# Kernel tuning notes

Hardware: AMD Instinct MI355X
Metric: run time of the kernel (lower is better)

The kernel has to match this reference:

```python
import jax, jax.numpy as jnp
import numpy as np

D_MODEL = 1024
N_HEADS = 16
LN_EPS = 1e-6  # flax LayerNorm default

def setup_inputs() -> dict:
    key = jax.random.key(0)
    k1, k2, k3 = jax.random.split(key, 3)
    B, S = 2, 2048
    x = jax.random.normal(k1, (B, S, D_MODEL), dtype=jnp.float32)
    W_qkv = jax.random.normal(k2, (D_MODEL, 3 * D_MODEL), dtype=jnp.float32) / np.sqrt(D_MODEL)
    W_out = jax.random.normal(k3, (D_MODEL, D_MODEL), dtype=jnp.float32) / np.sqrt(D_MODEL)
    q_scale = jnp.ones((D_MODEL,), dtype=jnp.float32)
    k_scale = jnp.ones((D_MODEL,), dtype=jnp.float32)
    return {"x": x, "W_qkv": W_qkv, "q_scale": q_scale, "k_scale": k_scale, "W_out": W_out}

def _layernorm(t, scale):
    mu = jnp.mean(t, axis=-1, keepdims=True)
    var = jnp.var(t, axis=-1, keepdims=True)
    return (t - mu) * jax.lax.rsqrt(var + LN_EPS) * scale

def reference(x, W_qkv, q_scale, k_scale, W_out):
    B, S, D = x.shape
    H = N_HEADS
    Hd = D // H
    # fused QKV projection (no bias)
    qkv = jnp.einsum('bsd,de->bse', x, W_qkv)
    q, k, v = jnp.split(qkv, 3, axis=-1)
    # QK-LayerNorm over full d_model (before head split), scale only
    q = _layernorm(q, q_scale)
    k = _layernorm(k, k_scale)
    # split heads: [b, s, h, hd]
    q = q.reshape(B, S, H, Hd)
    k = k.reshape(B, S, H, Hd)
    v = v.reshape(B, S, H, Hd)
    # eager attention with causal mask
    scores = jnp.einsum('bshd,bthd->bhst', q / jnp.sqrt(Hd).astype(q.dtype), k)  # [b,h,s,t]
    future = jnp.triu(jnp.ones((S, S), dtype=bool), 1)  # True on strictly-future positions
    scores = jnp.where(future[None, None, :, :], jnp.finfo(scores.dtype).min, scores)
    attn = jax.nn.softmax(scores, axis=-1)
    ctx = jnp.einsum('bhst,bthd->bshd', attn, v)
    out = jnp.einsum('bsd,de->bse', ctx.reshape(B, S, D), W_out)
    return out
```

## Files before the change

### kernel.cpp

```cpp
#include <hip/hip_runtime.h>
#include <cstdint>
#include <cstddef>

typedef __attribute__((ext_vector_type(8))) short short8;
typedef __attribute__((ext_vector_type(4))) float floatx4;

__device__ __forceinline__ float bf2f(unsigned short u) {
  union { unsigned int i; float f; } c; c.i = ((unsigned int)u) << 16; return c.f;
}
__device__ __forceinline__ unsigned short f2bf(float f) {
  union { float f; unsigned int i; } c; c.f = f;
  unsigned int r = c.i + 0x7fffu + ((c.i >> 16) & 1u);
  return (unsigned short)(r >> 16);
}
__device__ __forceinline__ unsigned int fbits(float f) {
  union { float f; unsigned int i; } c; c.f = f; return c.i;
}

__device__ __forceinline__ void glds16(const unsigned short* g, unsigned short* l) {
  __builtin_amdgcn_global_load_lds((const __attribute__((address_space(1))) void*)g,
                                   (__attribute__((address_space(3))) void*)l, 16, 0, 0);
}

__device__ __forceinline__ void tr_tile(const float* __restrict__ in,
                                        unsigned short* __restrict__ out,
                                        int R, int C, int bx, int by, int tid,
                                        unsigned short (*t)[33]) {
  const int cx = tid & 31, rl = tid >> 5;
#pragma unroll
  for (int i = 0; i < 4; ++i)
    t[rl + i * 8][cx] = f2bf(in[(size_t)(by * 32 + rl + i * 8) * C + bx * 32 + cx]);
  __syncthreads();
  const int oc = by * 32 + cx;
#pragma unroll
  for (int i = 0; i < 4; ++i)
    out[(size_t)(bx * 32 + rl + i * 8) * R + oc] = t[cx][rl + i * 8];
}

__global__ __launch_bounds__(256) void k_prep(const float* __restrict__ x,
                                              const float* __restrict__ Wq,
                                              const float* __restrict__ Wo,
                                              unsigned short* __restrict__ x_bf,
                                              unsigned short* __restrict__ WTq,
                                              unsigned short* __restrict__ WTo) {
  __shared__ unsigned short t[32][33];
  const int bid = blockIdx.x, tid = threadIdx.x;
  if (bid < 3072) {
    tr_tile(Wq, WTq, 1024, 3072, bid % 96, bid / 96, tid, t);
  } else if (bid < 4096) {
    int v = bid - 3072;
    tr_tile(Wo, WTo, 1024, 1024, v & 31, v >> 5, tid, t);
  } else {
    int i = (bid - 4096) * 256 + tid;
    float4 v = ((const float4*)x)[i];
    ushort4 o = { f2bf(v.x), f2bf(v.y), f2bf(v.z), f2bf(v.w) };
    ((ushort4*)x_bf)[i] = o;
  }
}

template <int MT, bool F32OUT>
__global__ __launch_bounds__(256) void k_gemm_bt(const unsigned short* __restrict__ A,
                                                 const unsigned short* __restrict__ BT,
                                                 void* __restrict__ Cout,
                                                 int M, int N, int K) {
  constexpr int NI = MT / 32;
  __shared__ unsigned short As[2][MT * 32];
  __shared__ unsigned short Bs[2][128 * 32];
  const int bm = blockIdx.x * MT, bn = blockIdx.y * 128;
  const int tid = threadIdx.x;
  const int wave = tid >> 6, lane = tid & 63;
  const int wm = (wave & 1) * (MT / 2), wn = (wave >> 1) * 64;
  const int lrow = lane & 15, lgrp = lane >> 4;
  floatx4 acc[NI][4] = {};

  const int lr4 = lane >> 2, lc8 = (lane & 3) * 8;
  const int br0 = wave * 32;
  const unsigned short* Bg0 = BT + (size_t)(bn + br0 + lr4) * K + lc8;
  const unsigned short* Bg1 = BT + (size_t)(bn + br0 + 16 + lr4) * K + lc8;
  const int ar0 = wave * (MT / 4);
  const unsigned short* Ag0 = A + (size_t)(bm + ar0 + lr4) * K + lc8;
  const unsigned short* Ag1 = A + (size_t)(bm + ar0 + 16 + lr4) * K + lc8;

  for (int k0 = 0; k0 < K; k0 += 64) {
#pragma unroll
    for (int u = 0; u < 2; ++u) {
      const int ko = k0 + u * 32;
      glds16(Ag0 + ko, &As[u][ar0 * 32]);
      if (MT == 128) glds16(Ag1 + ko, &As[u][(ar0 + 16) * 32]);
      glds16(Bg0 + ko, &Bs[u][br0 * 32]);
      glds16(Bg1 + ko, &Bs[u][(br0 + 16) * 32]);
    }
    __syncthreads();
#pragma unroll
    for (int u = 0; u < 2; ++u) {
      short8 a[NI], bfr[4];
#pragma unroll
      for (int i = 0; i < NI; ++i)
        a[i] = *(const short8*)&As[u][(wm + i * 16 + lrow) * 32 + lgrp * 8];
#pragma unroll
      for (int j = 0; j < 4; ++j)
        bfr[j] = *(const short8*)&Bs[u][(wn + j * 16 + lrow) * 32 + lgrp * 8];
#pragma unroll
      for (int i = 0; i < NI; ++i)
#pragma unroll
        for (int j = 0; j < 4; ++j)
          acc[i][j] = __builtin_amdgcn_mfma_f32_16x16x32_bf16(a[i], bfr[j], acc[i][j], 0, 0, 0);
    }
    __syncthreads();
  }
#pragma unroll
  for (int i = 0; i < NI; ++i)
#pragma unroll
    for (int j = 0; j < 4; ++j)
#pragma unroll
      for (int r = 0; r < 4; ++r) {
        int m = bm + wm + i * 16 + lgrp * 4 + r;
        int n = bn + wn + j * 16 + lrow;
        if (F32OUT)
          ((float*)Cout)[(size_t)m * N + n] = acc[i][j][r];
        else
          ((unsigned short*)Cout)[(size_t)m * N + n] = f2bf(acc[i][j][r]);
      }
}

__global__ __launch_bounds__(256) void k_lnv(const unsigned short* __restrict__ qkv,
                                             const float* __restrict__ q_scale,
                                             const float* __restrict__ k_scale,
                                             unsigned short* __restrict__ q_n,
                                             unsigned short* __restrict__ k_n,
                                             unsigned short* __restrict__ VT) {
  const int bid = blockIdx.x, tid = threadIdx.x;
  if (bid < 4096) {
    const int tok = bid;
    const int wave = tid >> 6, lane = tid & 63;
    __shared__ float red[2][4];
    const unsigned short* row = qkv + (size_t)tok * 3072;
#pragma unroll
    for (int seg = 0; seg < 2; ++seg) {
      const unsigned short* p  = row + seg * 1024;
      const float* sc = seg ? k_scale : q_scale;
      unsigned short* outp = (seg ? k_n : q_n) + (size_t)tok * 1024;
      ushort4 u = *(const ushort4*)&p[tid * 4];
      float xv[4] = { bf2f(u.x), bf2f(u.y), bf2f(u.z), bf2f(u.w) };
      float sum = xv[0] + xv[1] + xv[2] + xv[3];
      float sq  = xv[0]*xv[0] + xv[1]*xv[1] + xv[2]*xv[2] + xv[3]*xv[3];
      for (int off = 32; off; off >>= 1) {
        sum += __shfl_down(sum, off, 64);
        sq  += __shfl_down(sq,  off, 64);
      }
      if (lane == 0) { red[0][wave] = sum; red[1][wave] = sq; }
      __syncthreads();
      sum = red[0][0] + red[0][1] + red[0][2] + red[0][3];
      sq  = red[1][0] + red[1][1] + red[1][2] + red[1][3];
      __syncthreads();
      float mean = sum * (1.0f / 1024.0f);
      float var  = sq * (1.0f / 1024.0f) - mean * mean;
      float rstd = rsqrtf(var + 1e-6f);
      if (seg == 0) rstd *= 0.18033688011112042f;
      float4 su = *(const float4*)&sc[tid * 4];
      ushort4 o;
      o.x = f2bf((xv[0] - mean) * rstd * su.x);
      o.y = f2bf((xv[1] - mean) * rstd * su.y);
      o.z = f2bf((xv[2] - mean) * rstd * su.z);
      o.w = f2bf((xv[3] - mean) * rstd * su.w);
      *(ushort4*)&outp[tid * 4] = o;
    }
  } else {
    __shared__ unsigned short t[32][33];
    const int v = bid - 4096;
    const int bh = v & 31, b = bh >> 4, h = bh & 15;
    const int sy = (v >> 5) & 63, hx = v >> 11;
    const int cx = tid & 31, rl = tid >> 5;
#pragma unroll
    for (int i = 0; i < 4; ++i)
      t[rl + i * 8][cx] =
        qkv[(size_t)(b * 2048 + sy * 32 + rl + i * 8) * 3072 + 2048 + h * 64 + hx * 32 + cx];
    __syncthreads();
#pragma unroll
    for (int i = 0; i < 4; ++i)
      VT[((size_t)bh * 64 + hx * 32 + rl + i * 8) * 2048 + sy * 32 + cx] = t[cx][rl + i * 8];
  }
}


#define KS_STRIDE 72
#define VS_STRIDE 136
#define PS_STRIDE 136

#define MFMA_BF16 __builtin_amdgcn_mfma_f32_16x16x32_bf16

template <bool MASKED>
__device__ __forceinline__ void attn_step(int t0, int q0, int wq, int wt,
    const short8 (&qa)[2][2],
    const unsigned short* Ks, const unsigned short* Vs, unsigned short* Psq,
    floatx4 (&o)[2][4], floatx4 (&o_l)[2], int lrow, int lgrp) {
  const int twbase = wt * 64;
#pragma unroll
  for (int tb = 0; tb < 4; ++tb) {
    short8 kb0 = *(const short8*)&Ks[(twbase + tb * 16 + lrow) * KS_STRIDE + lgrp * 8];
    short8 kb1 = *(const short8*)&Ks[(twbase + tb * 16 + lrow) * KS_STRIDE + 32 + lgrp * 8];
#pragma unroll
    for (int qb = 0; qb < 2; ++qb) {
      floatx4 st = {};
      st = MFMA_BF16(kb0, qa[qb][0], st, 0, 0, 0);
      st = MFMA_BF16(kb1, qa[qb][1], st, 0, 0, 0);
      float p0 = exp2f(st[0]), p1 = exp2f(st[1]);
      float p2 = exp2f(st[2]), p3 = exp2f(st[3]);
      if (MASKED) {
        const int qcol = q0 + wq * 32 + qb * 16 + lrow;
        const int tbase = t0 + twbase + tb * 16 + lgrp * 4;
        p0 = (tbase     <= qcol) ? p0 : 0.0f;
        p1 = (tbase + 1 <= qcol) ? p1 : 0.0f;
        p2 = (tbase + 2 <= qcol) ? p2 : 0.0f;
        p3 = (tbase + 3 <= qcol) ? p3 : 0.0f;
      }
      uint2 pu;
      pu.x = __builtin_amdgcn_perm(fbits(p1), fbits(p0), 0x07060302u);
      pu.y = __builtin_amdgcn_perm(fbits(p3), fbits(p2), 0x07060302u);
      *(uint2*)&Psq[(qb * 16 + lrow) * PS_STRIDE + twbase + tb * 16 + lgrp * 4] = pu;
    }
  }
  const short8 vones = { 0x3F80, 0x3F80, 0x3F80, 0x3F80,
                         0x3F80, 0x3F80, 0x3F80, 0x3F80 };
#pragma unroll
  for (int kk = 0; kk < 2; ++kk) {
    short8 pa0 = *(const short8*)&Psq[lrow * PS_STRIDE + twbase + kk * 32 + lgrp * 8];
    short8 pa1 = *(const short8*)&Psq[(16 + lrow) * PS_STRIDE + twbase + kk * 32 + lgrp * 8];
    o_l[0] = MFMA_BF16(pa0, vones, o_l[0], 0, 0, 0);
    o_l[1] = MFMA_BF16(pa1, vones, o_l[1], 0, 0, 0);
#pragma unroll
    for (int hb = 0; hb < 4; ++hb) {
      short8 vb = *(const short8*)&Vs[(hb * 16 + lrow) * VS_STRIDE + twbase + kk * 32 + lgrp * 8];
      o[0][hb] = MFMA_BF16(pa0, vb, o[0][hb], 0, 0, 0);
      o[1][hb] = MFMA_BF16(pa1, vb, o[1][hb], 0, 0, 0);
    }
  }
}

__global__ __launch_bounds__(256) void k_flash(const unsigned short* __restrict__ q_n,
                                               const unsigned short* __restrict__ k_n,
                                               const unsigned short* __restrict__ VT,
                                               unsigned short* __restrict__ ctx) {
  const int S = 2048, D = 1024;
  const int bh = blockIdx.x, b = bh >> 4, h = bh & 15;
  const int qt = 31 - (int)blockIdx.y;
  const int q0 = qt * 64;
  const int tid = threadIdx.x, wave = tid >> 6, lane = tid & 63;
  const int wq = wave >> 1, wt = wave & 1;
  const int lrow = lane & 15, lgrp = lane >> 4;

  __shared__ __align__(16) unsigned char smem[53248];
  unsigned short* Ks  = (unsigned short*)smem;
  unsigned short* Vs  = (unsigned short*)(smem + 18432);
  unsigned short* Psq = (unsigned short*)(smem + 35840) + wq * 32 * PS_STRIDE;
  float* buf  = (float*)smem;
  float* Lbuf = (float*)(smem + 17408);

  const unsigned short* kg = k_n + (size_t)(b * S) * D + h * 64;
  const unsigned short* vg = VT + (size_t)bh * 64 * S;
  const int ksr = tid >> 3, ksc = (tid & 7) * 8;
  const int vsr = tid >> 4, vsc = (tid & 15) * 8;

  short8 qa[2][2];
#pragma unroll
  for (int qb = 0; qb < 2; ++qb) {
    const unsigned short* qp =
        q_n + (size_t)(b * S + q0 + wq * 32 + qb * 16 + lrow) * D + h * 64;
    qa[qb][0] = *(const short8*)(qp + lgrp * 8);
    qa[qb][1] = *(const short8*)(qp + 32 + lgrp * 8);
  }
  floatx4 o[2][4] = {};
  floatx4 o_l[2] = {};

  const int tend = q0 + 64;
  for (int t0 = 0; t0 < tend; t0 += 128) {
#pragma unroll
    for (int j = 0; j < 4; ++j) {
      int r = ksr + j * 32;
      *(int4*)&Ks[r * KS_STRIDE + ksc] = *(const int4*)(kg + (size_t)(t0 + r) * D + ksc);
    }
#pragma unroll
    for (int j = 0; j < 4; ++j) {
      int r = vsr + j * 16;
      *(int4*)&Vs[r * VS_STRIDE + vsc] = *(const int4*)(vg + (size_t)r * S + t0 + vsc);
    }
    __syncthreads();
    const bool half = (tend - t0) < 128;
    if (!(half && wt == 1)) {
      if (t0 + 128 <= q0)
        attn_step<false>(t0, q0, wq, wt, qa, Ks, Vs, Psq, o, o_l, lrow, lgrp);
      else
        attn_step<true>(t0, q0, wq, wt, qa, Ks, Vs, Psq, o, o_l, lrow, lgrp);
    }
    __syncthreads();
  }

  if (wt == 1) {
    if (lrow == 0) {
#pragma unroll
      for (int qb = 0; qb < 2; ++qb)
#pragma unroll
        for (int r = 0; r < 4; ++r)
          Lbuf[wq * 32 + qb * 16 + lgrp * 4 + r] = o_l[qb][r];
    }
    float* bf = buf + wq * 32 * 68;
#pragma unroll
    for (int qb = 0; qb < 2; ++qb)
#pragma unroll
      for (int hb = 0; hb < 4; ++hb)
#pragma unroll
        for (int r = 0; r < 4; ++r)
          bf[(qb * 16 + lgrp * 4 + r) * 68 + hb * 16 + lrow] = o[qb][hb][r];
  }
  __syncthreads();
  if (wt == 0) {
    float* bf = buf + wq * 32 * 68;
#pragma unroll
    for (int qb = 0; qb < 2; ++qb)
#pragma unroll
      for (int hb = 0; hb < 4; ++hb)
#pragma unroll
        for (int r = 0; r < 4; ++r)
          o[qb][hb][r] += bf[(qb * 16 + lgrp * 4 + r) * 68 + hb * 16 + lrow];
    unsigned short* op = ctx + (size_t)(b * S + q0 + wq * 32) * D + h * 64;
#pragma unroll
    for (int qb = 0; qb < 2; ++qb)
#pragma unroll
      for (int r = 0; r < 4; ++r) {
        float inv = 1.0f / (o_l[qb][r] + Lbuf[wq * 32 + qb * 16 + lgrp * 4 + r]);
        int row = qb * 16 + lgrp * 4 + r;
#pragma unroll
        for (int hb = 0; hb < 4; ++hb)
          op[(size_t)row * D + hb * 16 + lrow] = f2bf(o[qb][hb][r] * inv);
      }
  }
}

extern "C" void kernel_launch(void* const* d_in, const int* in_sizes, int n_in,
                              void* d_out, int out_size, void* d_ws, size_t ws_size,
                              hipStream_t stream) {
  const float* x       = (const float*)d_in[0];
  const float* W_qkv   = (const float*)d_in[1];
  const float* q_scale = (const float*)d_in[2];
  const float* k_scale = (const float*)d_in[3];
  const float* W_out   = (const float*)d_in[4];
  float* out = (float*)d_out;
  char* ws = (char*)d_ws;
  unsigned short* WT_qkv = (unsigned short*)(ws + 0);
  unsigned short* WT_out = (unsigned short*)(ws + 6291456);
  unsigned short* qkv    = (unsigned short*)(ws + 8388608);
  unsigned short* q_nb   = (unsigned short*)(ws + 33554432);
  unsigned short* k_nb   = (unsigned short*)(ws + 41943040);
  unsigned short* VT     = (unsigned short*)(ws + 50331648);
  unsigned short* x_bf   = (unsigned short*)(ws + 58720256);
  unsigned short* ctx    = qkv;

  k_prep<<<8192, 256, 0, stream>>>(x, W_qkv, W_out, x_bf, WT_qkv, WT_out);
  k_gemm_bt<128, false><<<dim3(32, 24), 256, 0, stream>>>(x_bf, WT_qkv, qkv, 4096, 3072, 1024);
  k_lnv<<<8192, 256, 0, stream>>>(qkv, q_scale, k_scale, q_nb, k_nb, VT);
  k_flash<<<dim3(32, 32), 256, 0, stream>>>(q_nb, k_nb, VT, ctx);
  k_gemm_bt<64, true><<<dim3(64, 8), 256, 0, stream>>>(ctx, WT_out, out, 4096, 1024, 1024);
}
```

Baseline: 183.7 us.

## Shrink flash attention KV tile to 64 and snake-order query tiles

The flash attention kernel now walks the key/value sequence in 64-wide tiles instead of 128. Each wave pair splits a 32-key half, which cuts shared memory from about 52KB to 27KB so more blocks can sit on each CU. It also removes the half-tile waste on the diagonal. The query-tile order across blockIdx.y becomes a serpentine mapping instead of longest-first, which changes how causal work is spread over the launch. The cost is twice as many barrier pairs and global load rounds per key range, with fewer MFMAs between syncs.

```diff
diff --git a/kernel.cpp b/kernel.cpp
--- a/kernel.cpp
+++ b/kernel.cpp
@@ -184,8 +184,8 @@
 
 
 #define KS_STRIDE 72
-#define VS_STRIDE 136
-#define PS_STRIDE 136
+#define VS_STRIDE 72
+#define PS_STRIDE 72
 
 #define MFMA_BF16 __builtin_amdgcn_mfma_f32_16x16x32_bf16
 
@@ -194,9 +194,9 @@
     const short8 (&qa)[2][2],
     const unsigned short* Ks, const unsigned short* Vs, unsigned short* Psq,
     floatx4 (&o)[2][4], floatx4 (&o_l)[2], int lrow, int lgrp) {
-  const int twbase = wt * 64;
-#pragma unroll
-  for (int tb = 0; tb < 4; ++tb) {
+  const int twbase = wt * 32;
+#pragma unroll
+  for (int tb = 0; tb < 2; ++tb) {
     short8 kb0 = *(const short8*)&Ks[(twbase + tb * 16 + lrow) * KS_STRIDE + lgrp * 8];
     short8 kb1 = *(const short8*)&Ks[(twbase + tb * 16 + lrow) * KS_STRIDE + 32 + lgrp * 8];
 #pragma unroll
@@ -222,18 +222,15 @@
   }
   const short8 vones = { 0x3F80, 0x3F80, 0x3F80, 0x3F80,
                          0x3F80, 0x3F80, 0x3F80, 0x3F80 };
-#pragma unroll
-  for (int kk = 0; kk < 2; ++kk) {
-    short8 pa0 = *(const short8*)&Psq[lrow * PS_STRIDE + twbase + kk * 32 + lgrp * 8];
-    short8 pa1 = *(const short8*)&Psq[(16 + lrow) * PS_STRIDE + twbase + kk * 32 + lgrp * 8];
-    o_l[0] = MFMA_BF16(pa0, vones, o_l[0], 0, 0, 0);
-    o_l[1] = MFMA_BF16(pa1, vones, o_l[1], 0, 0, 0);
-#pragma unroll
-    for (int hb = 0; hb < 4; ++hb) {
-      short8 vb = *(const short8*)&Vs[(hb * 16 + lrow) * VS_STRIDE + twbase + kk * 32 + lgrp * 8];
-      o[0][hb] = MFMA_BF16(pa0, vb, o[0][hb], 0, 0, 0);
-      o[1][hb] = MFMA_BF16(pa1, vb, o[1][hb], 0, 0, 0);
-    }
+  short8 pa0 = *(const short8*)&Psq[lrow * PS_STRIDE + twbase + lgrp * 8];
+  short8 pa1 = *(const short8*)&Psq[(16 + lrow) * PS_STRIDE + twbase + lgrp * 8];
+  o_l[0] = MFMA_BF16(pa0, vones, o_l[0], 0, 0, 0);
+  o_l[1] = MFMA_BF16(pa1, vones, o_l[1], 0, 0, 0);
+#pragma unroll
+  for (int hb = 0; hb < 4; ++hb) {
+    short8 vb = *(const short8*)&Vs[(hb * 16 + lrow) * VS_STRIDE + twbase + lgrp * 8];
+    o[0][hb] = MFMA_BF16(pa0, vb, o[0][hb], 0, 0, 0);
+    o[1][hb] = MFMA_BF16(pa1, vb, o[1][hb], 0, 0, 0);
   }
 }
 
@@ -243,23 +240,23 @@
                                                unsigned short* __restrict__ ctx) {
   const int S = 2048, D = 1024;
   const int bh = blockIdx.x, b = bh >> 4, h = bh & 15;
-  const int qt = 31 - (int)blockIdx.y;
+  const int byi = (int)blockIdx.y, bi = byi & 7, bj = byi >> 3;
+  const int qt = 8 * bj + ((bj & 1) ? (7 - bi) : bi);
   const int q0 = qt * 64;
   const int tid = threadIdx.x, wave = tid >> 6, lane = tid & 63;
   const int wq = wave >> 1, wt = wave & 1;
   const int lrow = lane & 15, lgrp = lane >> 4;
 
-  __shared__ __align__(16) unsigned char smem[53248];
+  __shared__ __align__(16) unsigned char smem[27648];
   unsigned short* Ks  = (unsigned short*)smem;
-  unsigned short* Vs  = (unsigned short*)(smem + 18432);
-  unsigned short* Psq = (unsigned short*)(smem + 35840) + wq * 32 * PS_STRIDE;
+  unsigned short* Vs  = (unsigned short*)(smem + 9216);
+  unsigned short* Psq = (unsigned short*)(smem + 18432) + wq * 32 * PS_STRIDE;
   float* buf  = (float*)smem;
   float* Lbuf = (float*)(smem + 17408);
 
   const unsigned short* kg = k_n + (size_t)(b * S) * D + h * 64;
   const unsigned short* vg = VT + (size_t)bh * 64 * S;
-  const int ksr = tid >> 3, ksc = (tid & 7) * 8;
-  const int vsr = tid >> 4, vsc = (tid & 15) * 8;
+  const int sr = tid >> 3, sc = (tid & 7) * 8;
 
   short8 qa[2][2];
 #pragma unroll
@@ -273,25 +270,16 @@
   floatx4 o_l[2] = {};
 
   const int tend = q0 + 64;
-  for (int t0 = 0; t0 < tend; t0 += 128) {
-#pragma unroll
-    for (int j = 0; j < 4; ++j) {
-      int r = ksr + j * 32;
-      *(int4*)&Ks[r * KS_STRIDE + ksc] = *(const int4*)(kg + (size_t)(t0 + r) * D + ksc);
-    }
-#pragma unroll
-    for (int j = 0; j < 4; ++j) {
-      int r = vsr + j * 16;
-      *(int4*)&Vs[r * VS_STRIDE + vsc] = *(const int4*)(vg + (size_t)r * S + t0 + vsc);
-    }
-    __syncthreads();
-    const bool half = (tend - t0) < 128;
-    if (!(half && wt == 1)) {
-      if (t0 + 128 <= q0)
-        attn_step<false>(t0, q0, wq, wt, qa, Ks, Vs, Psq, o, o_l, lrow, lgrp);
-      else
-        attn_step<true>(t0, q0, wq, wt, qa, Ks, Vs, Psq, o, o_l, lrow, lgrp);
-    }
+  for (int t0 = 0; t0 < tend; t0 += 64) {
+    *(int4*)&Ks[sr * KS_STRIDE + sc]        = *(const int4*)(kg + (size_t)(t0 + sr) * D + sc);
+    *(int4*)&Ks[(sr + 32) * KS_STRIDE + sc] = *(const int4*)(kg + (size_t)(t0 + sr + 32) * D + sc);
+    *(int4*)&Vs[sr * VS_STRIDE + sc]        = *(const int4*)(vg + (size_t)sr * S + t0 + sc);
+    *(int4*)&Vs[(sr + 32) * VS_STRIDE + sc] = *(const int4*)(vg + (size_t)(sr + 32) * S + t0 + sc);
+    __syncthreads();
+    if (t0 + 64 <= q0)
+      attn_step<false>(t0, q0, wq, wt, qa, Ks, Vs, Psq, o, o_l, lrow, lgrp);
+    else
+      attn_step<true>(t0, q0, wq, wt, qa, Ks, Vs, Psq, o, o_l, lrow, lgrp);
     __syncthreads();
   }
 
```

After: 194.6 us. 1.06x slower.
